# Optimization experiments

Measured on AMD Instinct MI355X. Metric: run time of the kernel, lower is better.

## Reference

```python
import jax, jax.numpy as jnp
import numpy as np

N_NODES = 100000
N_EDGES = 800000
D_IN = 128
D_HID = 128


def setup_inputs() -> dict:
    key = jax.random.key(0)
    ks = jax.random.split(key, 5)
    x = jax.random.normal(ks[0], (N_NODES, D_IN), dtype=jnp.float32)
    edge_index = jax.random.randint(ks[1], (2, N_EDGES), 0, N_NODES, dtype=jnp.int64)
    W1 = jax.random.normal(ks[2], (D_HID, D_IN), dtype=jnp.float32) * 0.05
    b1 = jnp.zeros((D_HID,), dtype=jnp.float32)
    W2 = jax.random.normal(ks[3], (D_HID, D_HID), dtype=jnp.float32) * 0.05
    b2 = jnp.zeros((D_HID,), dtype=jnp.float32)
    return {"x": x, "edge_index": edge_index, "W1": W1, "b1": b1, "W2": W2, "b2": b2}


def _gcn_conv(x, W, b, src, dst, norm, num_nodes):
    # x' = x @ W^T, then scatter-add normalized messages to dst, then + bias
    h = x @ W.T                                  # [N, d_out]
    msg = h[src] * norm[:, None]                 # [E+N, d_out] gather + scale
    out = jax.ops.segment_sum(msg, dst, num_segments=num_nodes)
    return out + b


def reference(x, edge_index, W1, b1, W2, b2):
    n = x.shape[0]
    loops = jnp.arange(n, dtype=edge_index.dtype)
    src = jnp.concatenate([edge_index[0], loops])  # self-loops appended (PyG GCNConv)
    dst = jnp.concatenate([edge_index[1], loops])
    # symmetric normalization: deg over target nodes (weight 1 per edge)
    deg = jax.ops.segment_sum(jnp.ones_like(dst, dtype=x.dtype), dst, num_segments=n)
    dis = jnp.where(deg > 0, jax.lax.rsqrt(jnp.maximum(deg, 1e-12)), 0.0)
    norm = dis[src] * dis[dst]
    h = jax.nn.relu(_gcn_conv(x, W1, b1, src, dst, norm, n))
    return _gcn_conv(h, W2, b2, src, dst, norm, n)
```

## Files before the change

kernel.cpp:

```cpp
#include <hip/hip_runtime.h>

#define D 128
#define BE 4096
#define SC 5120

typedef __attribute__((ext_vector_type(8))) short bf16x8;
typedef __attribute__((ext_vector_type(4))) float f32x4;
typedef __attribute__((ext_vector_type(8))) unsigned short u16x8;

__device__ inline unsigned short f2bf(float f) {
    unsigned u = __float_as_uint(f);
    return (unsigned short)((u + 0x7fff + ((u >> 16) & 1)) >> 16);
}
__device__ inline float bf2f(unsigned short s) {
    return __uint_as_float((unsigned)s << 16);
}
__device__ inline bf16x8 cvt8(const float* __restrict__ p) {
    float4 a = *(const float4*)p;
    float4 b = *(const float4*)(p + 4);
    bf16x8 r;
    r[0] = (short)f2bf(a.x); r[1] = (short)f2bf(a.y);
    r[2] = (short)f2bf(a.z); r[3] = (short)f2bf(a.w);
    r[4] = (short)f2bf(b.x); r[5] = (short)f2bf(b.y);
    r[6] = (short)f2bf(b.z); r[7] = (short)f2bf(b.w);
    return r;
}

__global__ void k_prep(const float* __restrict__ W1, const float* __restrict__ W2,
                       unsigned short* __restrict__ Wb1, unsigned short* __restrict__ Wb2,
                       int* __restrict__ bcnt, int* __restrict__ gcnt, int NBK) {
    int i = blockIdx.x * 256 + threadIdx.x;
    if (i < D * D) { Wb1[i] = f2bf(W1[i]); Wb2[i] = f2bf(W2[i]); }
    if (i < NBK) bcnt[i] = 0;
    if (i == D * D) *gcnt = 0;
}


template <bool INBF16, bool FOLD>
__device__ inline void gemm_tile(const void* __restrict__ in_v,
                                 const unsigned short* __restrict__ Wb,
                                 const int* __restrict__ cnt,
                                 unsigned short* __restrict__ g,
                                 int N, int tile, int t) {
    int w = t >> 6, l = t & 63;
    int r16 = l & 15, g4 = l >> 4;
    int base = tile * 128 + w * 32;
    int row0 = base + r16, row1 = row0 + 16;
    int cr0 = (row0 < N) ? row0 : N - 1;
    int cr1 = (row1 < N) ? row1 : N - 1;

    f32x4 acc0[8] = {};
    f32x4 acc1[8] = {};
    const unsigned short* wr = Wb + r16 * D + g4 * 8;

#pragma unroll 1
    for (int ks = 0; ks < 4; ks++) {
        bf16x8 b0, b1;
        if (INBF16) {
            const unsigned short* h = (const unsigned short*)in_v;
            b0 = *(const bf16x8*)(h + (size_t)cr0 * D + g4 * 8 + ks * 32);
            b1 = *(const bf16x8*)(h + (size_t)cr1 * D + g4 * 8 + ks * 32);
        } else {
            const float* xx = (const float*)in_v;
            b0 = cvt8(xx + (size_t)cr0 * D + g4 * 8 + ks * 32);
            b1 = cvt8(xx + (size_t)cr1 * D + g4 * 8 + ks * 32);
        }
#pragma unroll
        for (int jt = 0; jt < 8; jt++) {
            bf16x8 a = *(const bf16x8*)(wr + jt * 16 * D + ks * 32);
            acc0[jt] = __builtin_amdgcn_mfma_f32_16x16x32_bf16(a, b0, acc0[jt], 0, 0, 0);
            acc1[jt] = __builtin_amdgcn_mfma_f32_16x16x32_bf16(a, b1, acc1[jt], 0, 0, 0);
        }
    }
#pragma unroll
    for (int tt = 0; tt < 2; tt++) {
        int row = base + tt * 16 + r16;
        if (row < N) {
            float dv = 1.0f;
            if (FOLD) dv = rsqrtf((float)(cnt[row] + 1));
#pragma unroll
            for (int jt = 0; jt < 8; jt++) {
                f32x4 a = tt ? acc1[jt] : acc0[jt];
                ushort4 o = { f2bf(a[0] * dv), f2bf(a[1] * dv),
                              f2bf(a[2] * dv), f2bf(a[3] * dv) };
                *(ushort4*)&g[(size_t)row * D + jt * 16 + g4 * 4] = o;
            }
        }
    }
}


__global__ __launch_bounds__(256) void k_sort(
        const int* __restrict__ ei, int* __restrict__ bcnt, unsigned* __restrict__ brec,
        int E, int NBK) {
    __shared__ unsigned srt[BE];
    __shared__ unsigned char bko[BE];
    __shared__ int hist[256];
    __shared__ int pfx[256];
    __shared__ int gbase[256];
    __shared__ int cur[256];
    int t = threadIdx.x;
    int e0 = blockIdx.x * BE;
    int n = E - e0; if (n > BE) n = BE;

    hist[t] = 0; cur[t] = 0;
    __syncthreads();

    unsigned rec[16]; int mb[16];
#pragma unroll
    for (int j = 0; j < 16; j++) {
        int e = e0 + j * 256 + t;
        if (e < E) {
            int s = ei[e], d = ei[E + e];
            rec[j] = ((unsigned)s << 9) | (unsigned)(d & 511);
            mb[j] = d >> 9;
            atomicAdd(&hist[mb[j]], 1);
        } else mb[j] = -1;
    }
    __syncthreads();
    int v = hist[t];
    pfx[t] = v;
    __syncthreads();
    for (int dd = 1; dd < 256; dd <<= 1) {
        int xv = (t >= dd) ? pfx[t - dd] : 0;
        __syncthreads();
        pfx[t] += xv;
        __syncthreads();
    }
    pfx[t] -= v;
    if (v > 0 && t < NBK) gbase[t] = atomicAdd(&bcnt[t], v);
    __syncthreads();
#pragma unroll
    for (int j = 0; j < 16; j++) {
        if (mb[j] >= 0) {
            int p = pfx[mb[j]] + atomicAdd(&cur[mb[j]], 1);
            srt[p] = rec[j];
            bko[p] = (unsigned char)mb[j];
        }
    }
    __syncthreads();
    for (int i = t; i < n; i += 256) {
        int b = bko[i];
        int pos = gbase[b] + (i - pfx[b]);
        if (pos < SC) brec[(size_t)b * SC + pos] = srt[i];
    }
}


__global__ __launch_bounds__(256) void k_build_gemm1(
        const int* __restrict__ bcnt, const unsigned* __restrict__ brec,
        int* __restrict__ cnt, int* __restrict__ rp, int* __restrict__ col,
        int* __restrict__ gcnt,
        const float* __restrict__ x, const unsigned short* __restrict__ Wb1,
        unsigned short* __restrict__ g, int N, int ntiles, int NBK) {
    int bid = blockIdx.x;
    if (bid % 5 == 4) {
        __shared__ int c512[512];
        __shared__ int base512[512];
        __shared__ int psc[256];
        __shared__ int bksum;
        int b = bid / 5, t = threadIdx.x;
        if (b >= NBK) return;
        c512[t] = 0; c512[t + 256] = 0;
        __syncthreads();
        int total = bcnt[b]; if (total > SC) total = SC;
        for (int i = t; i < total; i += 256)
            atomicAdd(&c512[brec[(size_t)b * SC + i] & 511], 1);
        __syncthreads();
        int d0 = c512[2 * t], d1 = c512[2 * t + 1];
        int pair = d0 + d1;
        psc[t] = pair;
        __syncthreads();
        for (int dd = 1; dd < 256; dd <<= 1) {
            int xv = (t >= dd) ? psc[t - dd] : 0;
            __syncthreads();
            psc[t] += xv;
            __syncthreads();
        }
        int pexc = psc[t] - pair;
        if (t == 255) bksum = atomicAdd(gcnt, psc[255]);
        __syncthreads();
        int gb = bksum;
        base512[2 * t]     = gb + pexc;
        base512[2 * t + 1] = gb + pexc + d0;
        c512[2 * t] = 0; c512[2 * t + 1] = 0;
        __syncthreads();
        for (int i = t; i < total; i += 256) {
            unsigned rec = brec[(size_t)b * SC + i];
            int dl = rec & 511;
            int p = atomicAdd(&c512[dl], 1);
            col[base512[dl] + p] = (int)(rec >> 9);
        }
        __syncthreads();
#pragma unroll
        for (int k = 0; k < 2; k++) {
            int dl = t + k * 256;
            int node = b * 512 + dl;
            if (node < N) { cnt[node] = c512[dl]; rp[node] = base512[dl]; }
        }
    } else {
        int gid = (bid / 5) * 4 + (bid % 5);
        if (gid >= ntiles) return;
        gemm_tile<false, false>(x, Wb1, nullptr, g, N, gid, threadIdx.x);
    }
}

__global__ __launch_bounds__(256) void k_gemm2(
        const unsigned short* __restrict__ h, const unsigned short* __restrict__ Wb2,
        const int* __restrict__ cnt, unsigned short* __restrict__ g2, int N, int ntiles) {
    if ((int)blockIdx.x >= ntiles) return;
    gemm_tile<true, true>(h, Wb2, cnt, g2, N, blockIdx.x, threadIdx.x);
}


template <bool RELU, bool OUT_BF16, bool DISU>
__global__ __launch_bounds__(256) void k_agg(
        const unsigned short* __restrict__ gtab, const int* __restrict__ cnt,
        const int* __restrict__ rp, const int* __restrict__ col,
        const float* __restrict__ bias, void* __restrict__ out, int N) {
    int node = blockIdx.x * 16 + (threadIdx.x >> 4);
    if (node >= N) return;
    int l16 = threadIdx.x & 15;
    const u16x8* G = (const u16x8*)gtab;
    int deg = cnt[node];
    float disv = rsqrtf((float)(deg + 1));
    float acc[8];
    {
        u16x8 s = G[(size_t)node * 16 + l16];
        float sf = DISU ? disv : 1.0f;
#pragma unroll
        for (int j = 0; j < 8; j++) acc[j] = bf2f(s[j]) * sf;
    }
    const int* cb = col + rp[node];
    int i = 0;
    for (; i + 3 < deg; i += 4) {
        int u0 = cb[i], u1 = cb[i + 1], u2 = cb[i + 2], u3 = cb[i + 3];
        u16x8 m0 = G[(size_t)u0 * 16 + l16];
        u16x8 m1 = G[(size_t)u1 * 16 + l16];
        u16x8 m2 = G[(size_t)u2 * 16 + l16];
        u16x8 m3 = G[(size_t)u3 * 16 + l16];
        if (DISU) {
            float d0 = rsqrtf((float)(cnt[u0] + 1));
            float d1 = rsqrtf((float)(cnt[u1] + 1));
            float d2 = rsqrtf((float)(cnt[u2] + 1));
            float d3 = rsqrtf((float)(cnt[u3] + 1));
#pragma unroll
            for (int j = 0; j < 8; j++)
                acc[j] += (bf2f(m0[j]) * d0 + bf2f(m1[j]) * d1)
                        + (bf2f(m2[j]) * d2 + bf2f(m3[j]) * d3);
        } else {
#pragma unroll
            for (int j = 0; j < 8; j++)
                acc[j] += (bf2f(m0[j]) + bf2f(m1[j])) + (bf2f(m2[j]) + bf2f(m3[j]));
        }
    }
    for (; i < deg; i++) {
        int u = cb[i];
        u16x8 m = G[(size_t)u * 16 + l16];
        float du = DISU ? rsqrtf((float)(cnt[u] + 1)) : 1.0f;
#pragma unroll
        for (int j = 0; j < 8; j++) acc[j] += bf2f(m[j]) * du;
    }
    const float4* B4 = (const float4*)bias;
    float4 bb0 = B4[l16 * 2], bb1 = B4[l16 * 2 + 1];
    float r[8];
    r[0] = fmaf(acc[0], disv, bb0.x); r[1] = fmaf(acc[1], disv, bb0.y);
    r[2] = fmaf(acc[2], disv, bb0.z); r[3] = fmaf(acc[3], disv, bb0.w);
    r[4] = fmaf(acc[4], disv, bb1.x); r[5] = fmaf(acc[5], disv, bb1.y);
    r[6] = fmaf(acc[6], disv, bb1.z); r[7] = fmaf(acc[7], disv, bb1.w);
    if (RELU) {
#pragma unroll
        for (int j = 0; j < 8; j++) r[j] = fmaxf(r[j], 0.f);
    }
    if (OUT_BF16) {
        u16x8 o;
#pragma unroll
        for (int j = 0; j < 8; j++) o[j] = f2bf(r[j]);
        ((u16x8*)out)[(size_t)node * 16 + l16] = o;
    } else {
        float4 o0 = make_float4(r[0], r[1], r[2], r[3]);
        float4 o1 = make_float4(r[4], r[5], r[6], r[7]);
        ((float4*)out)[(size_t)node * 32 + l16 * 2]     = o0;
        ((float4*)out)[(size_t)node * 32 + l16 * 2 + 1] = o1;
    }
}


extern "C" void kernel_launch(void* const* d_in, const int* in_sizes, int n_in,
                              void* d_out, int out_size, void* d_ws, size_t ws_size,
                              hipStream_t stream) {
    const float* x  = (const float*)d_in[0];
    const int*   ei = (const int*)d_in[1];
    const float* W1 = (const float*)d_in[2];
    const float* b1 = (const float*)d_in[3];
    const float* W2 = (const float*)d_in[4];
    const float* b2 = (const float*)d_in[5];
    float* out = (float*)d_out;

    int N = in_sizes[0] / D;
    int E = in_sizes[1] / 2;
    int NBK = (N + 511) >> 9;

    char* w = (char*)d_ws;
    unsigned short* g  = (unsigned short*)w;  size_t off = (size_t)N * D * 2;
    off = (off + 255) & ~(size_t)255;
    unsigned short* g2 = (unsigned short*)(w + off); off += (size_t)N * D * 2;
    off = (off + 255) & ~(size_t)255;
    int* cnt  = (int*)(w + off);             off += (size_t)N * 4;
    off = (off + 255) & ~(size_t)255;
    int* rp   = (int*)(w + off);             off += (size_t)N * 4;
    off = (off + 255) & ~(size_t)255;
    int* col  = (int*)(w + off);             off += (size_t)E * 4;
    off = (off + 255) & ~(size_t)255;
    unsigned short* Wb1 = (unsigned short*)(w + off); off += (size_t)D * D * 2;
    unsigned short* Wb2 = (unsigned short*)(w + off); off += (size_t)D * D * 2;
    off = (off + 255) & ~(size_t)255;
    int* bcnt = (int*)(w + off);             off += (size_t)NBK * 4;
    off = (off + 255) & ~(size_t)255;
    int* gcnt = (int*)(w + off);             off += 256;
    unsigned* brec = (unsigned*)(w + off);   off += (size_t)NBK * SC * 4;
    unsigned short* h = (unsigned short*)d_out;

    int ntiles = (N + 127) / 128;
    int sortB  = (E + BE - 1) / BE;
    int fb = NBK > (ntiles + 3) / 4 ? NBK : (ntiles + 3) / 4;
    int total  = 5 * fb;
    int agg_grid = (N + 15) / 16;

    k_prep<<<(D * D + 511) / 256, 256, 0, stream>>>(W1, W2, Wb1, Wb2, bcnt, gcnt, NBK);

    k_sort<<<sortB, 256, 0, stream>>>(ei, bcnt, brec, E, NBK);

    k_build_gemm1<<<total, 256, 0, stream>>>(bcnt, brec, cnt, rp, col, gcnt,
                                             x, Wb1, g, N, ntiles, NBK);

    k_agg<true, true, true><<<agg_grid, 256, 0, stream>>>(g, cnt, rp, col, b1, h, N);

    k_gemm2<<<ntiles, 256, 0, stream>>>(h, Wb2, cnt, g2, N, ntiles);

    k_agg<false, false, false><<<agg_grid, 256, 0, stream>>>(g2, cnt, rp, col, b2, out, N);
}
```

Before: 161.6 us.

## Fuse layer-1 aggregation with GEMM2 and overlap sort with half of GEMM1

The edge sort kernel now also runs half of the GEMM1 tiles in interleaved blocks, and the CSR build kernel runs the other half, so bucketing and GEMM1 overlap. Layer-1 aggregation is fused with the second GEMM: each 16-node block writes its ReLU'd bf16 hidden rows into padded LDS and runs MFMA against W2 directly. This removes the h round trip through global memory and one launch. The cost is that each 16-row block reloads all of W2 from global or cache, and a tiny 16-row GEMM tile gives low MFMA utilisation.

```diff
diff --git a/kernel.cpp b/kernel.cpp
--- a/kernel.cpp
+++ b/kernel.cpp
@@ -3,6 +3,7 @@
 #define D 128
 #define BE 4096
 #define SC 5120
+#define LROW 136
 
 typedef __attribute__((ext_vector_type(8))) short bf16x8;
 typedef __attribute__((ext_vector_type(4))) float f32x4;
@@ -36,12 +37,10 @@
 }
 
 
-template <bool INBF16, bool FOLD>
-__device__ inline void gemm_tile(const void* __restrict__ in_v,
-                                 const unsigned short* __restrict__ Wb,
-                                 const int* __restrict__ cnt,
-                                 unsigned short* __restrict__ g,
-                                 int N, int tile, int t) {
+__device__ inline void gemm1_tile(const float* __restrict__ xx,
+                                  const unsigned short* __restrict__ Wb,
+                                  unsigned short* __restrict__ g,
+                                  int N, int tile, int t) {
     int w = t >> 6, l = t & 63;
     int r16 = l & 15, g4 = l >> 4;
     int base = tile * 128 + w * 32;
@@ -55,16 +54,8 @@
 
 #pragma unroll 1
     for (int ks = 0; ks < 4; ks++) {
-        bf16x8 b0, b1;
-        if (INBF16) {
-            const unsigned short* h = (const unsigned short*)in_v;
-            b0 = *(const bf16x8*)(h + (size_t)cr0 * D + g4 * 8 + ks * 32);
-            b1 = *(const bf16x8*)(h + (size_t)cr1 * D + g4 * 8 + ks * 32);
-        } else {
-            const float* xx = (const float*)in_v;
-            b0 = cvt8(xx + (size_t)cr0 * D + g4 * 8 + ks * 32);
-            b1 = cvt8(xx + (size_t)cr1 * D + g4 * 8 + ks * 32);
-        }
+        bf16x8 b0 = cvt8(xx + (size_t)cr0 * D + g4 * 8 + ks * 32);
+        bf16x8 b1 = cvt8(xx + (size_t)cr1 * D + g4 * 8 + ks * 32);
 #pragma unroll
         for (int jt = 0; jt < 8; jt++) {
             bf16x8 a = *(const bf16x8*)(wr + jt * 16 * D + ks * 32);
@@ -76,13 +67,10 @@
     for (int tt = 0; tt < 2; tt++) {
         int row = base + tt * 16 + r16;
         if (row < N) {
-            float dv = 1.0f;
-            if (FOLD) dv = rsqrtf((float)(cnt[row] + 1));
 #pragma unroll
             for (int jt = 0; jt < 8; jt++) {
                 f32x4 a = tt ? acc1[jt] : acc0[jt];
-                ushort4 o = { f2bf(a[0] * dv), f2bf(a[1] * dv),
-                              f2bf(a[2] * dv), f2bf(a[3] * dv) };
+                ushort4 o = { f2bf(a[0]), f2bf(a[1]), f2bf(a[2]), f2bf(a[3]) };
                 *(ushort4*)&g[(size_t)row * D + jt * 16 + g4 * 4] = o;
             }
         }
@@ -90,76 +78,83 @@
 }
 
 
-__global__ __launch_bounds__(256) void k_sort(
+__global__ __launch_bounds__(256) void k_sort_gemm1a(
         const int* __restrict__ ei, int* __restrict__ bcnt, unsigned* __restrict__ brec,
-        int E, int NBK) {
-    __shared__ unsigned srt[BE];
-    __shared__ unsigned char bko[BE];
-    __shared__ int hist[256];
-    __shared__ int pfx[256];
-    __shared__ int gbase[256];
-    __shared__ int cur[256];
-    int t = threadIdx.x;
-    int e0 = blockIdx.x * BE;
-    int n = E - e0; if (n > BE) n = BE;
-
-    hist[t] = 0; cur[t] = 0;
-    __syncthreads();
-
-    unsigned rec[16]; int mb[16];
-#pragma unroll
-    for (int j = 0; j < 16; j++) {
-        int e = e0 + j * 256 + t;
-        if (e < E) {
-            int s = ei[e], d = ei[E + e];
-            rec[j] = ((unsigned)s << 9) | (unsigned)(d & 511);
-            mb[j] = d >> 9;
-            atomicAdd(&hist[mb[j]], 1);
-        } else mb[j] = -1;
-    }
-    __syncthreads();
-    int v = hist[t];
-    pfx[t] = v;
-    __syncthreads();
-    for (int dd = 1; dd < 256; dd <<= 1) {
-        int xv = (t >= dd) ? pfx[t - dd] : 0;
-        __syncthreads();
-        pfx[t] += xv;
-        __syncthreads();
-    }
-    pfx[t] -= v;
-    if (v > 0 && t < NBK) gbase[t] = atomicAdd(&bcnt[t], v);
-    __syncthreads();
-#pragma unroll
-    for (int j = 0; j < 16; j++) {
-        if (mb[j] >= 0) {
-            int p = pfx[mb[j]] + atomicAdd(&cur[mb[j]], 1);
-            srt[p] = rec[j];
-            bko[p] = (unsigned char)mb[j];
-        }
-    }
-    __syncthreads();
-    for (int i = t; i < n; i += 256) {
-        int b = bko[i];
-        int pos = gbase[b] + (i - pfx[b]);
-        if (pos < SC) brec[(size_t)b * SC + pos] = srt[i];
-    }
-}
-
-
-__global__ __launch_bounds__(256) void k_build_gemm1(
+        const float* __restrict__ x, const unsigned short* __restrict__ Wb1,
+        unsigned short* __restrict__ g, int N, int E, int ntA, int sortB, int NBK) {
+    int bid = blockIdx.x;
+    if (bid % 3 == 2) {
+        __shared__ unsigned srt[BE];
+        __shared__ unsigned char bko[BE];
+        __shared__ int hist[256];
+        __shared__ int pfx[256];
+        __shared__ int gbase[256];
+        __shared__ int cur[256];
+        int f = bid / 3;
+        if (f >= sortB) return;
+        int t = threadIdx.x;
+        int e0 = f * BE;
+        int n = E - e0; if (n > BE) n = BE;
+        hist[t] = 0; cur[t] = 0;
+        __syncthreads();
+        unsigned rec[16]; int mb[16];
+#pragma unroll
+        for (int j = 0; j < 16; j++) {
+            int e = e0 + j * 256 + t;
+            if (e < E) {
+                int s = ei[e], d = ei[E + e];
+                rec[j] = ((unsigned)s << 9) | (unsigned)(d & 511);
+                mb[j] = d >> 9;
+                atomicAdd(&hist[mb[j]], 1);
+            } else mb[j] = -1;
+        }
+        __syncthreads();
+        int v = hist[t];
+        pfx[t] = v;
+        __syncthreads();
+        for (int dd = 1; dd < 256; dd <<= 1) {
+            int xv = (t >= dd) ? pfx[t - dd] : 0;
+            __syncthreads();
+            pfx[t] += xv;
+            __syncthreads();
+        }
+        pfx[t] -= v;
+        if (v > 0 && t < NBK) gbase[t] = atomicAdd(&bcnt[t], v);
+        __syncthreads();
+#pragma unroll
+        for (int j = 0; j < 16; j++) {
+            if (mb[j] >= 0) {
+                int p = pfx[mb[j]] + atomicAdd(&cur[mb[j]], 1);
+                srt[p] = rec[j];
+                bko[p] = (unsigned char)mb[j];
+            }
+        }
+        __syncthreads();
+        for (int i = t; i < n; i += 256) {
+            int b = bko[i];
+            int pos = gbase[b] + (i - pfx[b]);
+            if (pos < SC) brec[(size_t)b * SC + pos] = srt[i];
+        }
+    } else {
+        int gid = (bid / 3) * 2 + (bid % 3);
+        if (gid >= ntA) return;
+        gemm1_tile(x, Wb1, g, N, gid, threadIdx.x);
+    }
+}
+
+__global__ __launch_bounds__(256) void k_build_gemm1b(
         const int* __restrict__ bcnt, const unsigned* __restrict__ brec,
         int* __restrict__ cnt, int* __restrict__ rp, int* __restrict__ col,
         int* __restrict__ gcnt,
         const float* __restrict__ x, const unsigned short* __restrict__ Wb1,
-        unsigned short* __restrict__ g, int N, int ntiles, int NBK) {
+        unsigned short* __restrict__ g, int N, int ntA, int ntiles, int NBK) {
     int bid = blockIdx.x;
-    if (bid % 5 == 4) {
+    if (bid % 3 == 2) {
         __shared__ int c512[512];
         __shared__ int base512[512];
         __shared__ int psc[256];
         __shared__ int bksum;
-        int b = bid / 5, t = threadIdx.x;
+        int b = bid / 3, t = threadIdx.x;
         if (b >= NBK) return;
         c512[t] = 0; c512[t + 256] = 0;
         __syncthreads();
@@ -199,37 +194,113 @@
             if (node < N) { cnt[node] = c512[dl]; rp[node] = base512[dl]; }
         }
     } else {
-        int gid = (bid / 5) * 4 + (bid % 5);
+        int gid = ntA + (bid / 3) * 2 + (bid % 3);
         if (gid >= ntiles) return;
-        gemm_tile<false, false>(x, Wb1, nullptr, g, N, gid, threadIdx.x);
-    }
-}
-
-__global__ __launch_bounds__(256) void k_gemm2(
-        const unsigned short* __restrict__ h, const unsigned short* __restrict__ Wb2,
-        const int* __restrict__ cnt, unsigned short* __restrict__ g2, int N, int ntiles) {
-    if ((int)blockIdx.x >= ntiles) return;
-    gemm_tile<true, true>(h, Wb2, cnt, g2, N, blockIdx.x, threadIdx.x);
-}
-
-
-template <bool RELU, bool OUT_BF16, bool DISU>
-__global__ __launch_bounds__(256) void k_agg(
+        gemm1_tile(x, Wb1, g, N, gid, threadIdx.x);
+    }
+}
+
+
+__global__ __launch_bounds__(256) void k_agg1_g2(
         const unsigned short* __restrict__ gtab, const int* __restrict__ cnt,
         const int* __restrict__ rp, const int* __restrict__ col,
-        const float* __restrict__ bias, void* __restrict__ out, int N) {
+        const float* __restrict__ b1, const unsigned short* __restrict__ Wb2,
+        unsigned short* __restrict__ g2, int N) {
+    __shared__ __align__(16) unsigned short hl[16 * LROW];
+    int t = threadIdx.x, grp = t >> 4, l16 = t & 15;
+    int n0 = blockIdx.x * 16;
+    int node = n0 + grp;
+    bool valid = (node < N);
+    int nc = valid ? node : N - 1;
+    const u16x8* G = (const u16x8*)gtab;
+
+    int deg = valid ? cnt[node] : 0;
+    float disv = rsqrtf((float)(deg + 1));
+    float acc[8];
+    {
+        u16x8 s = G[(size_t)nc * 16 + l16];
+#pragma unroll
+        for (int j = 0; j < 8; j++) acc[j] = bf2f(s[j]) * disv;
+    }
+    const int* cb = col + (valid ? rp[node] : 0);
+    int i = 0;
+    for (; i + 3 < deg; i += 4) {
+        int u0 = cb[i], u1 = cb[i + 1], u2 = cb[i + 2], u3 = cb[i + 3];
+        u16x8 m0 = G[(size_t)u0 * 16 + l16];
+        u16x8 m1 = G[(size_t)u1 * 16 + l16];
+        u16x8 m2 = G[(size_t)u2 * 16 + l16];
+        u16x8 m3 = G[(size_t)u3 * 16 + l16];
+        float d0 = rsqrtf((float)(cnt[u0] + 1));
+        float d1 = rsqrtf((float)(cnt[u1] + 1));
+        float d2 = rsqrtf((float)(cnt[u2] + 1));
+        float d3 = rsqrtf((float)(cnt[u3] + 1));
+#pragma unroll
+        for (int j = 0; j < 8; j++)
+            acc[j] += (bf2f(m0[j]) * d0 + bf2f(m1[j]) * d1)
+                    + (bf2f(m2[j]) * d2 + bf2f(m3[j]) * d3);
+    }
+    for (; i < deg; i++) {
+        int u = cb[i];
+        u16x8 m = G[(size_t)u * 16 + l16];
+        float du = rsqrtf((float)(cnt[u] + 1));
+#pragma unroll
+        for (int j = 0; j < 8; j++) acc[j] += bf2f(m[j]) * du;
+    }
+    {
+        const float4* B4 = (const float4*)b1;
+        float4 bb0 = B4[l16 * 2], bb1 = B4[l16 * 2 + 1];
+        float r[8];
+        r[0] = fmaf(acc[0], disv, bb0.x); r[1] = fmaf(acc[1], disv, bb0.y);
+        r[2] = fmaf(acc[2], disv, bb0.z); r[3] = fmaf(acc[3], disv, bb0.w);
+        r[4] = fmaf(acc[4], disv, bb1.x); r[5] = fmaf(acc[5], disv, bb1.y);
+        r[6] = fmaf(acc[6], disv, bb1.z); r[7] = fmaf(acc[7], disv, bb1.w);
+        u16x8 hv;
+#pragma unroll
+        for (int j = 0; j < 8; j++)
+            hv[j] = valid ? f2bf(fmaxf(r[j], 0.f)) : (unsigned short)0;
+        *(u16x8*)&hl[grp * LROW + l16 * 8] = hv;
+    }
+    __syncthreads();
+
+    int w = t >> 6, l = t & 63;
+    int r16 = l & 15, g4 = l >> 4;
+    f32x4 a0 = {}, a1 = {};
+    const unsigned short* wr = Wb2 + r16 * D + g4 * 8;
+    int xb = r16 * LROW + g4 * 8;
+#pragma unroll 1
+    for (int ks = 0; ks < 4; ks++) {
+        bf16x8 b = *(const bf16x8*)&hl[xb + ks * 32];
+        bf16x8 A0 = *(const bf16x8*)(wr + (2 * w) * 16 * D + ks * 32);
+        bf16x8 A1 = *(const bf16x8*)(wr + (2 * w + 1) * 16 * D + ks * 32);
+        a0 = __builtin_amdgcn_mfma_f32_16x16x32_bf16(A0, b, a0, 0, 0, 0);
+        a1 = __builtin_amdgcn_mfma_f32_16x16x32_bf16(A1, b, a1, 0, 0, 0);
+    }
+    int orow = n0 + r16;
+    if (orow < N) {
+        float dv = rsqrtf((float)(cnt[orow] + 1));
+        ushort4 o0 = { f2bf(a0[0] * dv), f2bf(a0[1] * dv),
+                       f2bf(a0[2] * dv), f2bf(a0[3] * dv) };
+        ushort4 o1 = { f2bf(a1[0] * dv), f2bf(a1[1] * dv),
+                       f2bf(a1[2] * dv), f2bf(a1[3] * dv) };
+        *(ushort4*)&g2[(size_t)orow * D + (2 * w) * 16 + g4 * 4] = o0;
+        *(ushort4*)&g2[(size_t)orow * D + (2 * w + 1) * 16 + g4 * 4] = o1;
+    }
+}
+
+__global__ __launch_bounds__(256) void k_agg2(
+        const unsigned short* __restrict__ g2, const int* __restrict__ cnt,
+        const int* __restrict__ rp, const int* __restrict__ col,
+        const float* __restrict__ b2, float* __restrict__ out, int N) {
     int node = blockIdx.x * 16 + (threadIdx.x >> 4);
     if (node >= N) return;
     int l16 = threadIdx.x & 15;
-    const u16x8* G = (const u16x8*)gtab;
+    const u16x8* G = (const u16x8*)g2;
     int deg = cnt[node];
-    float disv = rsqrtf((float)(deg + 1));
     float acc[8];
     {
         u16x8 s = G[(size_t)node * 16 + l16];
-        float sf = DISU ? disv : 1.0f;
-#pragma unroll
-        for (int j = 0; j < 8; j++) acc[j] = bf2f(s[j]) * sf;
+#pragma unroll
+        for (int j = 0; j < 8; j++) acc[j] = bf2f(s[j]);
     }
     const int* cb = col + rp[node];
     int i = 0;
@@ -239,50 +310,25 @@
         u16x8 m1 = G[(size_t)u1 * 16 + l16];
         u16x8 m2 = G[(size_t)u2 * 16 + l16];
         u16x8 m3 = G[(size_t)u3 * 16 + l16];
-        if (DISU) {
-            float d0 = rsqrtf((float)(cnt[u0] + 1));
-            float d1 = rsqrtf((float)(cnt[u1] + 1));
-            float d2 = rsqrtf((float)(cnt[u2] + 1));
-            float d3 = rsqrtf((float)(cnt[u3] + 1));
-#pragma unroll
-            for (int j = 0; j < 8; j++)
-                acc[j] += (bf2f(m0[j]) * d0 + bf2f(m1[j]) * d1)
-                        + (bf2f(m2[j]) * d2 + bf2f(m3[j]) * d3);
-        } else {
-#pragma unroll
-            for (int j = 0; j < 8; j++)
-                acc[j] += (bf2f(m0[j]) + bf2f(m1[j])) + (bf2f(m2[j]) + bf2f(m3[j]));
-        }
+#pragma unroll
+        for (int j = 0; j < 8; j++)
+            acc[j] += (bf2f(m0[j]) + bf2f(m1[j])) + (bf2f(m2[j]) + bf2f(m3[j]));
     }
     for (; i < deg; i++) {
-        int u = cb[i];
-        u16x8 m = G[(size_t)u * 16 + l16];
-        float du = DISU ? rsqrtf((float)(cnt[u] + 1)) : 1.0f;
-#pragma unroll
-        for (int j = 0; j < 8; j++) acc[j] += bf2f(m[j]) * du;
-    }
-    const float4* B4 = (const float4*)bias;
+        u16x8 m = G[(size_t)cb[i] * 16 + l16];
+#pragma unroll
+        for (int j = 0; j < 8; j++) acc[j] += bf2f(m[j]);
+    }
+    float disv = rsqrtf((float)(deg + 1));
+    const float4* B4 = (const float4*)b2;
     float4 bb0 = B4[l16 * 2], bb1 = B4[l16 * 2 + 1];
-    float r[8];
-    r[0] = fmaf(acc[0], disv, bb0.x); r[1] = fmaf(acc[1], disv, bb0.y);
-    r[2] = fmaf(acc[2], disv, bb0.z); r[3] = fmaf(acc[3], disv, bb0.w);
-    r[4] = fmaf(acc[4], disv, bb1.x); r[5] = fmaf(acc[5], disv, bb1.y);
-    r[6] = fmaf(acc[6], disv, bb1.z); r[7] = fmaf(acc[7], disv, bb1.w);
-    if (RELU) {
-#pragma unroll
-        for (int j = 0; j < 8; j++) r[j] = fmaxf(r[j], 0.f);
-    }
-    if (OUT_BF16) {
-        u16x8 o;
-#pragma unroll
-        for (int j = 0; j < 8; j++) o[j] = f2bf(r[j]);
-        ((u16x8*)out)[(size_t)node * 16 + l16] = o;
-    } else {
-        float4 o0 = make_float4(r[0], r[1], r[2], r[3]);
-        float4 o1 = make_float4(r[4], r[5], r[6], r[7]);
-        ((float4*)out)[(size_t)node * 32 + l16 * 2]     = o0;
-        ((float4*)out)[(size_t)node * 32 + l16 * 2 + 1] = o1;
-    }
+    float4 o0, o1;
+    o0.x = fmaf(acc[0], disv, bb0.x); o0.y = fmaf(acc[1], disv, bb0.y);
+    o0.z = fmaf(acc[2], disv, bb0.z); o0.w = fmaf(acc[3], disv, bb0.w);
+    o1.x = fmaf(acc[4], disv, bb1.x); o1.y = fmaf(acc[5], disv, bb1.y);
+    o1.z = fmaf(acc[6], disv, bb1.z); o1.w = fmaf(acc[7], disv, bb1.w);
+    ((float4*)out)[(size_t)node * 32 + l16 * 2]     = o0;
+    ((float4*)out)[(size_t)node * 32 + l16 * 2 + 1] = o1;
 }
 
 
@@ -319,24 +365,23 @@
     off = (off + 255) & ~(size_t)255;
     int* gcnt = (int*)(w + off);             off += 256;
     unsigned* brec = (unsigned*)(w + off);   off += (size_t)NBK * SC * 4;
-    unsigned short* h = (unsigned short*)d_out;
 
     int ntiles = (N + 127) / 128;
-    int sortB  = (E + BE - 1) / BE;
-    int fb = NBK > (ntiles + 3) / 4 ? NBK : (ntiles + 3) / 4;
-    int total  = 5 * fb;
+    int ntA = (ntiles + 1) / 2;
+    int ntB = ntiles - ntA;
+    int sortB = (E + BE - 1) / BE;
+    int fb1 = sortB > (ntA + 1) / 2 ? sortB : (ntA + 1) / 2;
+    int fb2 = NBK   > (ntB + 1) / 2 ? NBK   : (ntB + 1) / 2;
     int agg_grid = (N + 15) / 16;
 
     k_prep<<<(D * D + 511) / 256, 256, 0, stream>>>(W1, W2, Wb1, Wb2, bcnt, gcnt, NBK);
 
-    k_sort<<<sortB, 256, 0, stream>>>(ei, bcnt, brec, E, NBK);
-
-    k_build_gemm1<<<total, 256, 0, stream>>>(bcnt, brec, cnt, rp, col, gcnt,
-                                             x, Wb1, g, N, ntiles, NBK);
-
-    k_agg<true, true, true><<<agg_grid, 256, 0, stream>>>(g, cnt, rp, col, b1, h, N);
-
-    k_gemm2<<<ntiles, 256, 0, stream>>>(h, Wb2, cnt, g2, N, ntiles);
-
-    k_agg<false, false, false><<<agg_grid, 256, 0, stream>>>(g2, cnt, rp, col, b2, out, N);
-}
+    k_sort_gemm1a<<<3 * fb1, 256, 0, stream>>>(ei, bcnt, brec, x, Wb1, g,
+                                               N, E, ntA, sortB, NBK);
+    k_build_gemm1b<<<3 * fb2, 256, 0, stream>>>(bcnt, brec, cnt, rp, col, gcnt,
+                                                x, Wb1, g, N, ntA, ntiles, NBK);
+
+    k_agg1_g2<<<agg_grid, 256, 0, stream>>>(g, cnt, rp, col, b1, Wb2, g2, N);
+
+    k_agg2<<<agg_grid, 256, 0, stream>>>(g2, cnt, rp, col, b2, out, N);
+}
```

Measured after the change: 160.0 us. About the same (-1.0%).
